# Kernel optimization log

Hardware: AMD Instinct MI355X
Metric: run time of the kernel (lower is better)

## Reference

```python
import jax, jax.numpy as jnp
import numpy as np

EMBED_DIM = 512
NUM_HEADS = 8
GAMMA = 0.1


def setup_inputs() -> dict:
    key = jax.random.key(0)
    ks = jax.random.split(key, 16)
    B, T, D, Hp, Wp = 4, 16, EMBED_DIM, 24, 24
    Dq = D // 4
    s = 1.0 / np.sqrt(D)
    inp = {
        "h_opt": jax.random.normal(ks[0], (B, T, D, Hp, Wp), jnp.float32),
        "h_sar": jax.random.normal(ks[1], (B, T, D, Hp, Wp), jnp.float32),
        "Wq": jax.random.normal(ks[2], (D, D), jnp.float32) * s,
        "bq": jnp.zeros((D,), jnp.float32),
        "Wk": jax.random.normal(ks[3], (D, D), jnp.float32) * s,
        "bk": jnp.zeros((D,), jnp.float32),
        "Wv": jax.random.normal(ks[4], (D, D), jnp.float32) * s,
        "bv": jnp.zeros((D,), jnp.float32),
        "Wo": jax.random.normal(ks[5], (D, D), jnp.float32) * s,
        "bo": jnp.zeros((D,), jnp.float32),
        "Wp1": jax.random.normal(ks[6], (D, Dq), jnp.float32) * s,
        "bp1": jnp.zeros((Dq,), jnp.float32),
        "Wp2": jax.random.normal(ks[7], (Dq, 1), jnp.float32) * (1.0 / np.sqrt(Dq)),
        "bp2": jnp.zeros((1,), jnp.float32),
    }
    return inp


def reference(h_opt, h_sar, Wq, bq, Wk, bk, Wv, bv, Wo, bo, Wp1, bp1, Wp2, bp2):
    B, T, D, Hp, Wp_ = h_opt.shape
    S = Hp * Wp_
    H = NUM_HEADS
    hd = D // H

    # (B,T,D,H',W') -> (B*S, T, D): each spatial location is an independent sequence over T
    opt_seq = jnp.transpose(h_opt, (0, 3, 4, 1, 2)).reshape(B * S, T, D)
    sar_seq = jnp.transpose(h_sar, (0, 3, 4, 1, 2)).reshape(B * S, T, D)

    Q = (opt_seq @ Wq + bq).reshape(B * S, T, H, hd)
    K = (sar_seq @ Wk + bk).reshape(B * S, T, H, hd)
    V = (sar_seq @ Wv + bv).reshape(B * S, T, H, hd)

    # scores: (N, H, Tq, Tk)
    scores = jnp.einsum("nthd,nshd->nhts", Q, K) / np.sqrt(hd).astype(np.float32)

    # per-key physical violation penalty: MLP(sar) -> sigmoid in [0,1], shape (N, Tk)
    hdn = jax.nn.gelu(sar_seq @ Wp1 + bp1, approximate=False)
    p_viol = jax.nn.sigmoid((hdn @ Wp2 + bp2).squeeze(-1))  # (N, T)
    scores = scores - GAMMA * p_viol[:, None, None, :]

    attn = jax.nn.softmax(scores, axis=-1)  # dropout is identity in eval mode
    out = jnp.einsum("nhts,nshd->nthd", attn, V).reshape(B * S, T, D)
    out = out @ Wo + bo
    return jnp.transpose(out.reshape(B, Hp, Wp_, T, D), (0, 3, 4, 1, 2))
```

## Files before the change

### kernel.cpp

```cpp
#include <hip/hip_runtime.h>

#define GAMMA 0.1f

typedef unsigned short u16;
typedef u16 u16x8 __attribute__((ext_vector_type(8)));
typedef short s16x8 __attribute__((ext_vector_type(8)));
typedef float f32x4 __attribute__((ext_vector_type(4)));
typedef unsigned int ui32x4 __attribute__((ext_vector_type(4)));
typedef unsigned int ui32x2 __attribute__((ext_vector_type(2)));

__device__ __forceinline__ float b2f(u16 u) {
  return __uint_as_float(((unsigned)u) << 16);
}
__device__ __forceinline__ u16 f2bf(float f) {
  unsigned u = __float_as_uint(f);
  unsigned r = (u + 0x7FFFu + ((u >> 16) & 1u)) >> 16;
  return (u16)r;
}
__device__ __forceinline__ unsigned pk_bf16(float lo, float hi) {
  return (unsigned)f2bf(lo) | ((unsigned)f2bf(hi) << 16);
}

__device__ __forceinline__ void gl2lds16(const u16* g, u16* l) {
  __builtin_amdgcn_global_load_lds(
      (const __attribute__((address_space(1))) unsigned int*)g,
      (__attribute__((address_space(3))) unsigned int*)l, 16, 0, 0);
}

__device__ __forceinline__ int xcd_swz(int phys, int nwg) {
  return (phys & 7) * (nwg >> 3) + (phys >> 3);
}

#define PREP_NCONV 9216
#define PREP_T0 9216
#define PREP_T1 10240
#define PREP_T2 11264
#define PREP_T3 12288
#define PREP_T4 12544
#define PREP_T5 13568
#define PREP_NB 13577

__device__ __forceinline__ void tr_block(
    const float* __restrict__ src, u16* __restrict__ dst, int N, int blk, int tid)
{
  int idx = blk * 256 + tid;
  int nn = idx >> 9, kk = idx & 511;
  dst[idx] = f2bf(src[kk * N + nn]);
}

__global__ __launch_bounds__(256) void prep_all(
    const float* __restrict__ h0, const float* __restrict__ h1,
    u16* __restrict__ d0, u16* __restrict__ d1,
    const float* __restrict__ Wq, const float* __restrict__ Wk,
    const float* __restrict__ Wv, const float* __restrict__ Wp1,
    const float* __restrict__ Wo,
    const float* __restrict__ bq, const float* __restrict__ bk,
    const float* __restrict__ bv, const float* __restrict__ bp1,
    const float* __restrict__ bo,
    u16* __restrict__ WqT, u16* __restrict__ KVPW, u16* __restrict__ WoT,
    float* __restrict__ biasQ, float* __restrict__ biasKVP,
    float* __restrict__ biasO)
{
  __shared__ __align__(16) u16 T[64 * 64];
  const int b = blockIdx.x;
  const int tid = threadIdx.x;

  if (b < PREP_NCONV) {
    const int z = b / 4608;
    const int r_ = b - z * 4608;
    const int bt = r_ / 72;
    const int xx = r_ - bt * 72;
    const int kt = xx & 7, st = xx >> 3;
    const float* src = (z ? h1 : h0) + (size_t)bt * (512 * 576);
    u16* dst = (z ? d1 : d0) + (size_t)bt * (576 * 512);

    const int s4 = (tid & 15) * 4;
    const int kq = (tid >> 4) * 4;
    const float* sp = src + (size_t)(kt * 64 + kq) * 576 + st * 64 + s4;
    float4 f0 = *(const float4*)(sp);
    float4 f1 = *(const float4*)(sp + 576);
    float4 f2 = *(const float4*)(sp + 1152);
    float4 f3 = *(const float4*)(sp + 1728);
    const int oc = kq >> 3;
    const int half = (kq >> 2) & 1;
    float a0[4] = {f0.x, f0.y, f0.z, f0.w};
    float a1[4] = {f1.x, f1.y, f1.z, f1.w};
    float a2[4] = {f2.x, f2.y, f2.z, f2.w};
    float a3[4] = {f3.x, f3.y, f3.z, f3.w};
#pragma unroll
    for (int i = 0; i < 4; ++i) {
      int s = s4 + i;
      ui32x2 q = {pk_bf16(a0[i], a1[i]), pk_bf16(a2[i], a3[i])};
      *(ui32x2*)&T[s * 64 + ((oc ^ (s & 7)) * 8) + half * 4] = q;
    }
    __syncthreads();
    const int r = tid >> 2, oc2 = (tid & 3) * 2;
    ui32x4 w0 = *(const ui32x4*)&T[r * 64 + ((oc2       ^ (r & 7)) * 8)];
    ui32x4 w1 = *(const ui32x4*)&T[r * 64 + (((oc2 + 1) ^ (r & 7)) * 8)];
    u16* dp = dst + (size_t)(st * 64 + r) * 512 + kt * 64 + oc2 * 8;
    *(ui32x4*)dp = w0;
    *(ui32x4*)(dp + 8) = w1;
  } else if (b < PREP_T1) {
    tr_block(Wq, WqT, 512, b - PREP_T0, tid);
  } else if (b < PREP_T2) {
    tr_block(Wk, KVPW, 512, b - PREP_T1, tid);
  } else if (b < PREP_T3) {
    tr_block(Wv, KVPW + 512 * 512, 512, b - PREP_T2, tid);
  } else if (b < PREP_T4) {
    tr_block(Wp1, KVPW + 1024 * 512, 128, b - PREP_T3, tid);
  } else if (b < PREP_T5) {
    tr_block(Wo, WoT, 512, b - PREP_T4, tid);
  } else {
    int i = (b - PREP_T5) * 256 + tid;
    if (i < 512) {
      biasQ[i] = bq[i];
    } else if (i < 1664) {
      int j = i - 512;
      float v;
      if (j < 512) v = bk[j];
      else if (j < 1024) v = bv[j - 512];
      else v = bp1[j - 1024];
      biasKVP[j] = v;
    } else if (i < 2176) {
      biasO[i - 1664] = bo[i - 1664];
    }
  }
}

__global__ __launch_bounds__(256) void gemm_proj_all(
    const u16* __restrict__ hTopt, const u16* __restrict__ hTsar,
    const u16* __restrict__ WqT, const u16* __restrict__ KVPW,
    const float* __restrict__ biasQ, const float* __restrict__ biasKVP,
    const float* __restrict__ Wp2, const float* __restrict__ bp2,
    u16* __restrict__ Qbuf, u16* __restrict__ KVPbuf,
    float* __restrict__ pviol)
{
  __shared__ __align__(16) u16 Al[2][64 * 64];
  __shared__ __align__(16) u16 Bl[2][128 * 64];
  __shared__ float Pv[256];
  const int tid = threadIdx.x;
  const int w = tid >> 6, lane = tid & 63;
  const int lhi = lane >> 4, llo = lane & 15;

  const int nwg = 13 * 576;
  const int phys = blockIdx.y * 13 + blockIdx.x;
  const int logical = xcd_swz(phys, nwg);
  const int bx = logical % 13;
  const int y = logical / 13;

  const int bt = y / 9, stile = y - bt * 9;
  const int s0 = stile * 64;

  const bool isQ = (bx < 4);
  const int bxl = isQ ? bx : bx - 4;
  const int col0 = bxl * 128;
  const int NC = isQ ? 512 : 1152;
  const u16* Ab = (isQ ? hTopt : hTsar) + (size_t)bt * (576 * 512)
                  + (size_t)s0 * 512;
  const u16* Bb = (isQ ? WqT : KVPW) + (size_t)col0 * 512;
  const float* bias = isQ ? biasQ : biasKVP;
  u16* C = isQ ? Qbuf : KVPbuf;
  const bool dopv = (!isQ) && (bxl == 8);

  const int brow = lane >> 3;
  const int bko = ((lane & 7) ^ brow) * 8;

  f32x4 acc[4][2];
#pragma unroll
  for (int mi = 0; mi < 4; ++mi)
#pragma unroll
    for (int ni = 0; ni < 2; ++ni)
#pragma unroll
      for (int e = 0; e < 4; ++e) acc[mi][ni][e] = 0.f;

#pragma unroll
  for (int i = 0; i < 2; ++i) {
    int q = w * 2 + i;
    gl2lds16(Ab + (size_t)(q * 8 + brow) * 512 + bko, &Al[0][q * 512]);
  }
#pragma unroll
  for (int i = 0; i < 4; ++i) {
    int q = w * 4 + i;
    gl2lds16(Bb + (size_t)(q * 8 + brow) * 512 + bko, &Bl[0][q * 512]);
  }

  for (int kt = 0; kt < 8; ++kt) {
    __syncthreads();
    if (kt < 7) {
      const int ktn = kt + 1;
#pragma unroll
      for (int i = 0; i < 2; ++i) {
        int q = w * 2 + i;
        gl2lds16(Ab + (size_t)(q * 8 + brow) * 512 + ktn * 64 + bko,
                 &Al[ktn & 1][q * 512]);
      }
#pragma unroll
      for (int i = 0; i < 4; ++i) {
        int q = w * 4 + i;
        gl2lds16(Bb + (size_t)(q * 8 + brow) * 512 + ktn * 64 + bko,
                 &Bl[ktn & 1][q * 512]);
      }
    }
    const u16* Alc = Al[kt & 1];
    const u16* Blc = Bl[kt & 1];
#pragma unroll
    for (int hh = 0; hh < 2; ++hh) {
      s16x8 af[4], bfr[2];
#pragma unroll
      for (int mi = 0; mi < 4; ++mi) {
        int row = mi * 16 + llo;
        af[mi] = *(const s16x8*)&Alc[row * 64 + ((((hh << 2) | lhi) ^ (row & 7)) * 8)];
      }
#pragma unroll
      for (int ni = 0; ni < 2; ++ni) {
        int n = w * 32 + ni * 16 + llo;
        bfr[ni] = *(const s16x8*)&Blc[n * 64 + ((((hh << 2) | lhi) ^ (n & 7)) * 8)];
      }
#pragma unroll
      for (int mi = 0; mi < 4; ++mi)
#pragma unroll
        for (int ni = 0; ni < 2; ++ni)
          acc[mi][ni] = __builtin_amdgcn_mfma_f32_16x16x32_bf16(
              af[mi], bfr[ni], acc[mi][ni], 0, 0, 0);
    }
  }

  const int b_ = bt >> 4, t_ = bt & 15;
  const size_t rowbase = (size_t)(b_ * 576 + s0) * 16 + t_;
  float bia0 = bias[col0 + w * 32 + llo];
  float bia1 = bias[col0 + w * 32 + 16 + llo];

  if (dopv) {
    const float w2a = Wp2[w * 32 + llo];
    const float w2b = Wp2[w * 32 + 16 + llo];
    float part[16];
#pragma unroll
    for (int mi = 0; mi < 4; ++mi)
#pragma unroll
      for (int i = 0; i < 4; ++i) {
        float x0 = acc[mi][0][i] + bia0;
        float x1 = acc[mi][1][i] + bia1;
        float g0 = 0.5f * x0 * (1.f + erff(x0 * 0.70710678f));
        float g1 = 0.5f * x1 * (1.f + erff(x1 * 0.70710678f));
        part[mi * 4 + i] = g0 * w2a + g1 * w2b;
      }
#pragma unroll
    for (int d = 1; d < 16; d <<= 1)
#pragma unroll
      for (int idx = 0; idx < 16; ++idx)
        part[idx] += __shfl_xor(part[idx], d, 64);
    if (llo == 0) {
#pragma unroll
      for (int mi = 0; mi < 4; ++mi)
#pragma unroll
        for (int i = 0; i < 4; ++i)
          Pv[w * 64 + mi * 16 + lhi * 4 + i] = part[mi * 4 + i];
    }
    __syncthreads();
    if (tid < 64) {
      float sum = Pv[tid] + Pv[64 + tid] + Pv[128 + tid] + Pv[192 + tid]
                  + bp2[0];
      pviol[rowbase + (size_t)tid * 16] = 1.f / (1.f + expf(-sum));
    }
  } else {
#pragma unroll
    for (int mi = 0; mi < 4; ++mi) {
#pragma unroll
      for (int i = 0; i < 4; ++i) {
        const int m = mi * 16 + lhi * 4 + i;
        u16* cp = C + (rowbase + (size_t)m * 16) * NC + col0 + w * 32 + llo;
        cp[0]  = f2bf(acc[mi][0][i] + bia0);
        cp[16] = f2bf(acc[mi][1][i] + bia1);
      }
    }
  }
}

__global__ __launch_bounds__(256) void attn_kernel(
    const u16* Q, const u16* __restrict__ KVP,
    const float* __restrict__ pviol, u16* att)
{
  __shared__ __align__(16) u16 Vl[4][16 * 72];
  __shared__ __align__(16) u16 Ol[4][16 * 72];
  const int tid = threadIdx.x;
  const int w = tid >> 6, lane = tid & 63;
  const int logical = xcd_swz(blockIdx.x, gridDim.x);
  const int wid = logical * 4 + w;
  const int n = wid >> 3, hh = wid & 7;
  const int g = lane >> 4, llo = lane & 15;

  const int r = lane >> 3, co = (lane & 7) * 8;
  {
    const u16* Vb = KVP + (size_t)n * (16 * 1152) + 512 + hh * 64;
#pragma unroll
    for (int rr = 0; rr < 2; ++rr) {
      int row = r + rr * 8;
      *(u16x8*)&Vl[w][row * 72 + co] =
          *(const u16x8*)(Vb + (size_t)row * 1152 + co);
    }
  }

  const u16* Qr = Q + ((size_t)n * 16 + llo) * 512 + hh * 64;
  const u16* Kr = KVP + ((size_t)n * 16 + llo) * 1152 + hh * 64;
  s16x8 qa0 = *(const s16x8*)(Qr + g * 8);
  s16x8 qa1 = *(const s16x8*)(Qr + 32 + g * 8);
  s16x8 ka0 = *(const s16x8*)(Kr + g * 8);
  s16x8 ka1 = *(const s16x8*)(Kr + 32 + g * 8);

  f32x4 sacc = {0.f, 0.f, 0.f, 0.f};
  sacc = __builtin_amdgcn_mfma_f32_16x16x32_bf16(ka0, qa0, sacc, 0, 0, 0);
  sacc = __builtin_amdgcn_mfma_f32_16x16x32_bf16(ka1, qa1, sacc, 0, 0, 0);

  const float* pv = pviol + n * 16;
  float s[4];
#pragma unroll
  for (int i = 0; i < 4; ++i) s[i] = sacc[i] * 0.125f - GAMMA * pv[g * 4 + i];

  float mx = fmaxf(fmaxf(s[0], s[1]), fmaxf(s[2], s[3]));
  mx = fmaxf(mx, __shfl_xor(mx, 16, 64));
  mx = fmaxf(mx, __shfl_xor(mx, 32, 64));
  float e[4], sum = 0.f;
#pragma unroll
  for (int i = 0; i < 4; ++i) { e[i] = expf(s[i] - mx); sum += e[i]; }
  sum += __shfl_xor(sum, 16, 64);
  sum += __shfl_xor(sum, 32, 64);
  float inv = 1.f / sum;

  unsigned p01 = pk_bf16(e[0] * inv, e[1] * inv);
  unsigned p23 = pk_bf16(e[2] * inv, e[3] * inv);

  const int sa = ((2 * g) & 3) * 16 + llo;
  const int sb = ((2 * g + 1) & 3) * 16 + llo;
  unsigned a0 = (unsigned)__shfl((int)p01, sa, 64);
  unsigned a1 = (unsigned)__shfl((int)p23, sa, 64);
  unsigned b0 = (unsigned)__shfl((int)p01, sb, 64);
  unsigned b1 = (unsigned)__shfl((int)p23, sb, 64);
  ui32x4 afu = {0u, 0u, 0u, 0u};
  if (g < 2) { afu[0] = a0; afu[1] = a1; afu[2] = b0; afu[3] = b1; }
  s16x8 pfrag;
  __builtin_memcpy(&pfrag, &afu, 16);

  f32x4 oacc[4];
#pragma unroll
  for (int c = 0; c < 4; ++c) {
    u16 vb[8];
#pragma unroll
    for (int j = 0; j < 8; ++j)
      vb[j] = (g < 2) ? Vl[w][(g * 8 + j) * 72 + c * 16 + llo] : (u16)0;
    s16x8 vfrag;
    __builtin_memcpy(&vfrag, vb, 16);
    f32x4 z = {0.f, 0.f, 0.f, 0.f};
    oacc[c] = __builtin_amdgcn_mfma_f32_16x16x32_bf16(pfrag, vfrag, z, 0, 0, 0);
  }

#pragma unroll
  for (int c = 0; c < 4; ++c)
#pragma unroll
    for (int i = 0; i < 4; ++i)
      Ol[w][(g * 4 + i) * 72 + c * 16 + llo] = f2bf(oacc[c][i]);

  {
    u16* ob = att + ((size_t)n * 16) * 512 + hh * 64;
#pragma unroll
    for (int rr = 0; rr < 2; ++rr) {
      int row = r + rr * 8;
      *(u16x8*)(ob + (size_t)row * 512 + co) = *(const u16x8*)&Ol[w][row * 72 + co];
    }
  }
}

__global__ __launch_bounds__(256) void gemm_out(
    const u16* __restrict__ A, const u16* __restrict__ WT,
    const float* __restrict__ bias, float* __restrict__ out)
{
  __shared__ __align__(16) char smem[49152];
  u16* Al0 = (u16*)smem;
  u16* Bl0 = (u16*)(smem + 16384);
  const int tid = threadIdx.x;
  const int w = tid >> 6, lane = tid & 63;
  const int lhi = lane >> 4, llo = lane & 15;

  const int nwg = gridDim.x * gridDim.y;
  const int phys = blockIdx.y * gridDim.x + blockIdx.x;
  const int logical = xcd_swz(phys, nwg);
  const int bx = logical % gridDim.x;
  const int y = logical / gridDim.x;

  const int bt = y / 9, stile = y - bt * 9;
  const int s0 = stile * 64;
  const int col0 = bx * 128;
  const int b_ = bt >> 4, t_ = bt & 15;

  const u16* Ab = A + ((size_t)(b_ * 576 + s0) * 16 + t_) * 512;
  const u16* Bb = WT + (size_t)col0 * 512;

  const int brow = lane >> 3;
  const int bko = ((lane & 7) ^ brow) * 8;

  f32x4 acc[4][2];
#pragma unroll
  for (int mi = 0; mi < 4; ++mi)
#pragma unroll
    for (int ni = 0; ni < 2; ++ni)
#pragma unroll
      for (int e = 0; e < 4; ++e) acc[mi][ni][e] = 0.f;

#pragma unroll
  for (int i = 0; i < 2; ++i) {
    int q = w * 2 + i;
    gl2lds16(Ab + (size_t)(q * 8 + brow) * (16 * 512) + bko, &Al0[q * 512]);
  }
#pragma unroll
  for (int i = 0; i < 4; ++i) {
    int q = w * 4 + i;
    gl2lds16(Bb + (size_t)(q * 8 + brow) * 512 + bko, &Bl0[q * 512]);
  }

  for (int kt = 0; kt < 8; ++kt) {
    __syncthreads();
    if (kt < 7) {
      const int ktn = kt + 1;
      u16* Ala = Al0 + (ktn & 1) * (64 * 64);
      u16* Bla = Bl0 + (ktn & 1) * (128 * 64);
#pragma unroll
      for (int i = 0; i < 2; ++i) {
        int q = w * 2 + i;
        gl2lds16(Ab + (size_t)(q * 8 + brow) * (16 * 512) + ktn * 64 + bko,
                 &Ala[q * 512]);
      }
#pragma unroll
      for (int i = 0; i < 4; ++i) {
        int q = w * 4 + i;
        gl2lds16(Bb + (size_t)(q * 8 + brow) * 512 + ktn * 64 + bko,
                 &Bla[q * 512]);
      }
    }
    const u16* Alc = Al0 + (kt & 1) * (64 * 64);
    const u16* Blc = Bl0 + (kt & 1) * (128 * 64);
#pragma unroll
    for (int hh = 0; hh < 2; ++hh) {
      s16x8 af[4], bfr[2];
#pragma unroll
      for (int mi = 0; mi < 4; ++mi) {
        int row = mi * 16 + llo;
        af[mi] = *(const s16x8*)&Alc[row * 64 + ((((hh << 2) | lhi) ^ (row & 7)) * 8)];
      }
#pragma unroll
      for (int ni = 0; ni < 2; ++ni) {
        int n = w * 32 + ni * 16 + llo;
        bfr[ni] = *(const s16x8*)&Blc[n * 64 + ((((hh << 2) | lhi) ^ (n & 7)) * 8)];
      }
#pragma unroll
      for (int mi = 0; mi < 4; ++mi)
#pragma unroll
        for (int ni = 0; ni < 2; ++ni)
          acc[mi][ni] = __builtin_amdgcn_mfma_f32_16x16x32_bf16(
              af[mi], bfr[ni], acc[mi][ni], 0, 0, 0);
    }
  }

  __syncthreads();
  float* Cl = (float*)smem;
  float bia0 = bias[col0 + w * 32 + llo];
  float bia1 = bias[col0 + w * 32 + 16 + llo];
#pragma unroll
  for (int mi = 0; mi < 4; ++mi)
#pragma unroll
    for (int i = 0; i < 4; ++i) {
      int m = mi * 16 + lhi * 4 + i;
      Cl[(w * 32 + llo) * 72 + m]      = acc[mi][0][i] + bia0;
      Cl[(w * 32 + 16 + llo) * 72 + m] = acc[mi][1][i] + bia1;
    }
  __syncthreads();
  const int nn = tid >> 1;
  const int mh = (tid & 1) * 32;
  const float* sp = Cl + nn * 72 + mh;
  float* dp = out + ((size_t)bt * 512 + col0 + nn) * 576 + s0 + mh;
#pragma unroll
  for (int j = 0; j < 8; ++j)
    *(float4*)(dp + j * 4) = *(const float4*)(sp + j * 4);
}

extern "C" void kernel_launch(void* const* d_in, const int* in_sizes, int n_in,
                              void* d_out, int out_size, void* d_ws, size_t ws_size,
                              hipStream_t stream)
{
  const float* h_opt = (const float*)d_in[0];
  const float* h_sar = (const float*)d_in[1];
  const float* Wq  = (const float*)d_in[2];
  const float* bq  = (const float*)d_in[3];
  const float* Wk  = (const float*)d_in[4];
  const float* bk  = (const float*)d_in[5];
  const float* Wv  = (const float*)d_in[6];
  const float* bv  = (const float*)d_in[7];
  const float* Wo  = (const float*)d_in[8];
  const float* bo  = (const float*)d_in[9];
  const float* Wp1 = (const float*)d_in[10];
  const float* bp1 = (const float*)d_in[11];
  const float* Wp2 = (const float*)d_in[12];
  const float* bp2 = (const float*)d_in[13];
  float* out = (float*)d_out;

  char* ws = (char*)d_ws;
  u16*   WqT     = (u16*)(ws + 0);
  u16*   KVPW    = (u16*)(ws + 524288);
  u16*   WoT     = (u16*)(ws + 1703936);
  float* biasQ   = (float*)(ws + 2228224);
  float* biasKVP = (float*)(ws + 2230272);
  float* biasO   = (float*)(ws + 2234880);
  float* pviol   = (float*)(ws + 2236928);
  u16*   Qbuf    = (u16*)(ws + 2384384);
  u16*   KVPbuf  = (u16*)(ws + 40133120);
  u16*   hTopt   = (u16*)(ws + 125067776);
  u16*   hTsar   = (u16*)(ws + 162816512);

  prep_all<<<PREP_NB, 256, 0, stream>>>(
      h_opt, h_sar, hTopt, hTsar, Wq, Wk, Wv, Wp1, Wo,
      bq, bk, bv, bp1, bo, WqT, KVPW, WoT, biasQ, biasKVP, biasO);

  gemm_proj_all<<<dim3(13, 576), 256, 0, stream>>>(
      hTopt, hTsar, WqT, KVPW, biasQ, biasKVP, Wp2, bp2,
      Qbuf, KVPbuf, pviol);

  attn_kernel<<<4608, 256, 0, stream>>>(Qbuf, KVPbuf, pviol, Qbuf);
  gemm_out<<<dim3(4, 576), 256, 0, stream>>>(Qbuf, WoT, biasO, out);
}
```

Baseline: 377.4 us.

## Enlarge projection GEMM tile to 128x128 with 8 waves per block

The projection GEMM block now covers 128 rows (two consecutive bt slices of 64 spatial rows) by 128 columns using 512 threads in a 4x2 wave grid, where before it covered 64x128 with 256 threads. Each B (weight) tile loaded into LDS is now reused across twice as many A rows, halving weight traffic per output and halving the grid size. The p_viol reduction and output row mapping are reworked for the split rows. Costs are more LDS per block (64KB) and fewer blocks, which may lower occupancy.

```diff
diff --git a/kernel.cpp b/kernel.cpp
--- a/kernel.cpp
+++ b/kernel.cpp
@@ -127,7 +127,7 @@
   }
 }
 
-__global__ __launch_bounds__(256) void gemm_proj_all(
+__global__ __launch_bounds__(512) void gemm_proj_all(
     const u16* __restrict__ hTopt, const u16* __restrict__ hTsar,
     const u16* __restrict__ WqT, const u16* __restrict__ KVPW,
     const float* __restrict__ biasQ, const float* __restrict__ biasKVP,
@@ -135,28 +135,31 @@
     u16* __restrict__ Qbuf, u16* __restrict__ KVPbuf,
     float* __restrict__ pviol)
 {
-  __shared__ __align__(16) u16 Al[2][64 * 64];
+  __shared__ __align__(16) u16 Al[2][128 * 64];
   __shared__ __align__(16) u16 Bl[2][128 * 64];
-  __shared__ float Pv[256];
+  __shared__ float Pv[2][128];
   const int tid = threadIdx.x;
   const int w = tid >> 6, lane = tid & 63;
   const int lhi = lane >> 4, llo = lane & 15;
-
-  const int nwg = 13 * 576;
+  const int wr = w >> 1, wc = w & 1;
+
+  const int nwg = 13 * 288;
   const int phys = blockIdx.y * 13 + blockIdx.x;
   const int logical = xcd_swz(phys, nwg);
   const int bx = logical % 13;
   const int y = logical / 13;
 
-  const int bt = y / 9, stile = y - bt * 9;
+  const int btp = y / 9, stile = y - btp * 9;
+  const int bt0 = btp * 2;
   const int s0 = stile * 64;
 
   const bool isQ = (bx < 4);
   const int bxl = isQ ? bx : bx - 4;
   const int col0 = bxl * 128;
   const int NC = isQ ? 512 : 1152;
-  const u16* Ab = (isQ ? hTopt : hTsar) + (size_t)bt * (576 * 512)
-                  + (size_t)s0 * 512;
+  const u16* hT = isQ ? hTopt : hTsar;
+  const u16* Ab0 = hT + (size_t)bt0 * (576 * 512) + (size_t)s0 * 512;
+  const u16* Ab1 = Ab0 + (size_t)(576 * 512);
   const u16* Bb = (isQ ? WqT : KVPW) + (size_t)col0 * 512;
   const float* bias = isQ ? biasQ : biasKVP;
   u16* C = isQ ? Qbuf : KVPbuf;
@@ -165,22 +168,23 @@
   const int brow = lane >> 3;
   const int bko = ((lane & 7) ^ brow) * 8;
 
-  f32x4 acc[4][2];
-#pragma unroll
-  for (int mi = 0; mi < 4; ++mi)
-#pragma unroll
-    for (int ni = 0; ni < 2; ++ni)
+  f32x4 acc[2][4];
+#pragma unroll
+  for (int mi = 0; mi < 2; ++mi)
+#pragma unroll
+    for (int ni = 0; ni < 4; ++ni)
 #pragma unroll
       for (int e = 0; e < 4; ++e) acc[mi][ni][e] = 0.f;
 
 #pragma unroll
   for (int i = 0; i < 2; ++i) {
     int q = w * 2 + i;
-    gl2lds16(Ab + (size_t)(q * 8 + brow) * 512 + bko, &Al[0][q * 512]);
-  }
-#pragma unroll
-  for (int i = 0; i < 4; ++i) {
-    int q = w * 4 + i;
+    const u16* Abase = (q < 8 ? Ab0 : Ab1) + (size_t)((q & 7) * 8 + brow) * 512;
+    gl2lds16(Abase + bko, &Al[0][q * 512]);
+  }
+#pragma unroll
+  for (int i = 0; i < 2; ++i) {
+    int q = w * 2 + i;
     gl2lds16(Bb + (size_t)(q * 8 + brow) * 512 + bko, &Bl[0][q * 512]);
   }
 
@@ -191,12 +195,12 @@
 #pragma unroll
       for (int i = 0; i < 2; ++i) {
         int q = w * 2 + i;
-        gl2lds16(Ab + (size_t)(q * 8 + brow) * 512 + ktn * 64 + bko,
-                 &Al[ktn & 1][q * 512]);
-      }
-#pragma unroll
-      for (int i = 0; i < 4; ++i) {
-        int q = w * 4 + i;
+        const u16* Abase = (q < 8 ? Ab0 : Ab1) + (size_t)((q & 7) * 8 + brow) * 512;
+        gl2lds16(Abase + ktn * 64 + bko, &Al[ktn & 1][q * 512]);
+      }
+#pragma unroll
+      for (int i = 0; i < 2; ++i) {
+        int q = w * 2 + i;
         gl2lds16(Bb + (size_t)(q * 8 + brow) * 512 + ktn * 64 + bko,
                  &Bl[ktn & 1][q * 512]);
       }
@@ -205,72 +209,86 @@
     const u16* Blc = Bl[kt & 1];
 #pragma unroll
     for (int hh = 0; hh < 2; ++hh) {
-      s16x8 af[4], bfr[2];
-#pragma unroll
-      for (int mi = 0; mi < 4; ++mi) {
-        int row = mi * 16 + llo;
+      s16x8 af[2], bfr[4];
+#pragma unroll
+      for (int mi = 0; mi < 2; ++mi) {
+        int row = wr * 32 + mi * 16 + llo;
         af[mi] = *(const s16x8*)&Alc[row * 64 + ((((hh << 2) | lhi) ^ (row & 7)) * 8)];
       }
 #pragma unroll
-      for (int ni = 0; ni < 2; ++ni) {
-        int n = w * 32 + ni * 16 + llo;
+      for (int ni = 0; ni < 4; ++ni) {
+        int n = wc * 64 + ni * 16 + llo;
         bfr[ni] = *(const s16x8*)&Blc[n * 64 + ((((hh << 2) | lhi) ^ (n & 7)) * 8)];
       }
 #pragma unroll
-      for (int mi = 0; mi < 4; ++mi)
-#pragma unroll
-        for (int ni = 0; ni < 2; ++ni)
+      for (int mi = 0; mi < 2; ++mi)
+#pragma unroll
+        for (int ni = 0; ni < 4; ++ni)
           acc[mi][ni] = __builtin_amdgcn_mfma_f32_16x16x32_bf16(
               af[mi], bfr[ni], acc[mi][ni], 0, 0, 0);
     }
   }
 
-  const int b_ = bt >> 4, t_ = bt & 15;
-  const size_t rowbase = (size_t)(b_ * 576 + s0) * 16 + t_;
-  float bia0 = bias[col0 + w * 32 + llo];
-  float bia1 = bias[col0 + w * 32 + 16 + llo];
+  const int b0_ = bt0 >> 4, t0_ = bt0 & 15;
+  const int bt1 = bt0 + 1;
+  const int b1_ = bt1 >> 4, t1_ = bt1 & 15;
+  const size_t rowbase0 = (size_t)(b0_ * 576 + s0) * 16 + t0_;
+  const size_t rowbase1 = (size_t)(b1_ * 576 + s0) * 16 + t1_;
+
+  float bia[4];
+#pragma unroll
+  for (int ni = 0; ni < 4; ++ni)
+    bia[ni] = bias[col0 + wc * 64 + ni * 16 + llo];
 
   if (dopv) {
-    const float w2a = Wp2[w * 32 + llo];
-    const float w2b = Wp2[w * 32 + 16 + llo];
-    float part[16];
-#pragma unroll
-    for (int mi = 0; mi < 4; ++mi)
+    float w2[4];
+#pragma unroll
+    for (int ni = 0; ni < 4; ++ni) w2[ni] = Wp2[wc * 64 + ni * 16 + llo];
+    float part[8];
+#pragma unroll
+    for (int mi = 0; mi < 2; ++mi)
 #pragma unroll
       for (int i = 0; i < 4; ++i) {
-        float x0 = acc[mi][0][i] + bia0;
-        float x1 = acc[mi][1][i] + bia1;
-        float g0 = 0.5f * x0 * (1.f + erff(x0 * 0.70710678f));
-        float g1 = 0.5f * x1 * (1.f + erff(x1 * 0.70710678f));
-        part[mi * 4 + i] = g0 * w2a + g1 * w2b;
+        float sum = 0.f;
+#pragma unroll
+        for (int ni = 0; ni < 4; ++ni) {
+          float x = acc[mi][ni][i] + bia[ni];
+          float gg = 0.5f * x * (1.f + erff(x * 0.70710678f));
+          sum += gg * w2[ni];
+        }
+        part[mi * 4 + i] = sum;
       }
 #pragma unroll
     for (int d = 1; d < 16; d <<= 1)
 #pragma unroll
-      for (int idx = 0; idx < 16; ++idx)
+      for (int idx = 0; idx < 8; ++idx)
         part[idx] += __shfl_xor(part[idx], d, 64);
     if (llo == 0) {
 #pragma unroll
-      for (int mi = 0; mi < 4; ++mi)
+      for (int mi = 0; mi < 2; ++mi)
 #pragma unroll
         for (int i = 0; i < 4; ++i)
-          Pv[w * 64 + mi * 16 + lhi * 4 + i] = part[mi * 4 + i];
+          Pv[wc][wr * 32 + mi * 16 + lhi * 4 + i] = part[mi * 4 + i];
     }
     __syncthreads();
-    if (tid < 64) {
-      float sum = Pv[tid] + Pv[64 + tid] + Pv[128 + tid] + Pv[192 + tid]
-                  + bp2[0];
-      pviol[rowbase + (size_t)tid * 16] = 1.f / (1.f + expf(-sum));
+    if (tid < 128) {
+      float sum = Pv[0][tid] + Pv[1][tid] + bp2[0];
+      size_t rb = (tid < 64) ? (rowbase0 + (size_t)tid * 16)
+                             : (rowbase1 + (size_t)(tid - 64) * 16);
+      pviol[rb] = 1.f / (1.f + expf(-sum));
     }
   } else {
 #pragma unroll
-    for (int mi = 0; mi < 4; ++mi) {
+    for (int mi = 0; mi < 2; ++mi) {
 #pragma unroll
       for (int i = 0; i < 4; ++i) {
-        const int m = mi * 16 + lhi * 4 + i;
-        u16* cp = C + (rowbase + (size_t)m * 16) * NC + col0 + w * 32 + llo;
-        cp[0]  = f2bf(acc[mi][0][i] + bia0);
-        cp[16] = f2bf(acc[mi][1][i] + bia1);
+        const int rloc = wr * 32 + mi * 16 + lhi * 4 + i;
+        const size_t crow = (rloc < 64 ? rowbase0 + (size_t)rloc * 16
+                                       : rowbase1 + (size_t)(rloc - 64) * 16);
+        u16* cp = C + crow * NC + col0 + wc * 64 + llo;
+#pragma unroll
+        for (int ni = 0; ni < 4; ++ni)
+          cp[ni * 16] = f2bf(acc[mi][ni][i] + bia[ni]);
       }
     }
   }
@@ -518,7 +536,7 @@
       h_opt, h_sar, hTopt, hTsar, Wq, Wk, Wv, Wp1, Wo,
       bq, bk, bv, bp1, bo, WqT, KVPW, WoT, biasQ, biasKVP, biasO);
 
-  gemm_proj_all<<<dim3(13, 576), 256, 0, stream>>>(
+  gemm_proj_all<<<dim3(13, 288), 512, 0, stream>>>(
       hTopt, hTsar, WqT, KVPW, biasQ, biasKVP, Wp2, bp2,
       Qbuf, KVPbuf, pviol);
 
```

Result: faster. 360.0 us (-4.6%).
